# Optimization experiments

Hardware: AMD Instinct MI355X
Metric: run time of the kernel (lower is better)

The kernel has to match this reference:

```python
import jax, jax.numpy as jnp
import numpy as np

B, S, D, H = 4, 1024, 1024, 16
DH = D // H
K_SPARSE = 32
LAMBDA_MAX, ALPHA = 10.0, 5.0
SPARSE_THRESHOLD = 1.0


def setup_inputs() -> dict:
    key = jax.random.key(0)
    ks = jax.random.split(key, 12)
    x = jax.random.normal(ks[0], (B, S, D), dtype=jnp.float32)
    prior_mask = jax.random.bernoulli(ks[1], 0.1, (S, S))
    prior_indices = jax.random.randint(ks[2], (S, K_SPARSE), 0, S)
    prior_index_mask = jax.random.bernoulli(ks[3], 0.9, (S, K_SPARSE))
    prior_index_mask = prior_index_mask.at[:, 0].set(True)  # avoid all-masked rows
    u_prev = jax.random.normal(ks[4], (B, 1), dtype=jnp.float32)
    sc = 1.0 / np.sqrt(D)
    Wq = jax.random.normal(ks[5], (D, D), dtype=jnp.float32) * sc
    Wk = jax.random.normal(ks[6], (D, D), dtype=jnp.float32) * sc
    Wv = jax.random.normal(ks[7], (D, D), dtype=jnp.float32) * sc
    Wo = jax.random.normal(ks[8], (D, D), dtype=jnp.float32) * sc
    bq = jnp.zeros((D,), jnp.float32)
    bk = jnp.zeros((D,), jnp.float32)
    bv = jnp.zeros((D,), jnp.float32)
    bo = jnp.zeros((D,), jnp.float32)
    return {"x": x, "prior_mask": prior_mask, "prior_indices": prior_indices,
            "prior_index_mask": prior_index_mask, "u_prev": u_prev,
            "Wq": Wq, "bq": bq, "Wk": Wk, "bk": bk, "Wv": Wv, "bv": bv,
            "Wo": Wo, "bo": bo}


def reference(x, prior_mask, prior_indices, prior_index_mask, u_prev,
              Wq, bq, Wk, bk, Wv, bv, Wo, bo):
    Bb, Ss, Dd = x.shape
    scale = 1.0 / jnp.sqrt(jnp.asarray(DH, x.dtype))

    def proj(W, b):
        return (x @ W.T + b).reshape(Bb, Ss, H, DH).transpose(0, 2, 1, 3)  # [B,H,S,DH]

    Q, K, V = proj(Wq, bq), proj(Wk, bk), proj(Wv, bv)

    lam = LAMBDA_MAX * jnp.exp(-ALPHA * u_prev.reshape(Bb))  # [B]
    use_sparse = lam >= SPARSE_THRESHOLD                      # [B] bool

    # ---- dense branch: full SDPA with lambda-scaled prior bias ----
    scores = jnp.einsum('bhqd,bhkd->bhqk', Q, K) * scale      # [B,H,S,S]
    prior_bias = jnp.where(prior_mask[:Ss, :Ss], 0.0, -1.0).astype(x.dtype)
    bias = lam[:, None, None, None] * prior_bias[None, None]
    dense_out = jnp.einsum('bhqk,bhkd->bhqd',
                           jax.nn.softmax(scores + bias, axis=-1), V)

    # ---- sparse branch: gather-indexed SDPA over prior_indices ----
    idx = prior_indices[:Ss]                                   # [S,k]
    Kg = K[:, :, idx]                                          # [B,H,S,k,DH]
    Vg = V[:, :, idx]
    s_scores = jnp.einsum('bhsd,bhskd->bhsk', Q, Kg) * scale   # [B,H,S,k]
    s_scores = jnp.where(prior_index_mask[:Ss][None, None], s_scores,
                         jnp.asarray(-jnp.inf, x.dtype))
    sparse_out = jnp.einsum('bhsk,bhskd->bhsd',
                            jax.nn.softmax(s_scores, axis=-1), Vg)

    out = jnp.where(use_sparse[:, None, None, None], sparse_out, dense_out)
    out = out.transpose(0, 2, 1, 3).reshape(Bb, Ss, Dd)
    return out @ Wo.T + bo
```

## Files before the change

### kernel.cpp

```cpp
#include <hip/hip_runtime.h>
#include <hip/hip_bf16.h>
#include <cmath>

#define NB 4
#define NS 1024
#define ND 1024
#define NH 16
#define NDH 64
#define NKSP 32
#define SCALE 0.125f
#define LOG2E 1.44269504f
#define SCALE2 (SCALE * LOG2E)

typedef __attribute__((ext_vector_type(8))) short bf16x8;
typedef __attribute__((ext_vector_type(4))) float f32x4;
typedef unsigned long long u64;

#define AS1 __attribute__((address_space(1)))
#define AS3 __attribute__((address_space(3)))

__device__ __forceinline__ void gl_lds16(const void* g, void* l) {
    __builtin_amdgcn_global_load_lds((const AS1 void*)g, (AS3 void*)l, 16, 0, 0);
}

__device__ __forceinline__ ushort f2bf(float f) {
    union { __hip_bfloat16 h; ushort u; } cv;
    cv.h = __float2bfloat16(f);
    return cv.u;
}
__device__ __forceinline__ float bf2f(ushort u) {
    union { unsigned int i; float f; } cv;
    cv.i = ((unsigned int)u) << 16;
    return cv.f;
}
__device__ __forceinline__ float fexp2(float x) {
    return __builtin_amdgcn_exp2f(x);
}

__global__ __launch_bounds__(256)
void f2bf_multi(const float* __restrict__ x,
                const float* __restrict__ w0, const float* __restrict__ w1,
                const float* __restrict__ w2, const float* __restrict__ w3,
                const int* __restrict__ pm,
                ushort* __restrict__ xo,
                ushort* __restrict__ o0, ushort* __restrict__ o1,
                ushort* __restrict__ o2, ushort* __restrict__ o3,
                u64* __restrict__ bm)
{
    int y = blockIdx.y;
    if (y == 5) {
        int word = blockIdx.x * 4 + (threadIdx.x >> 6);
        int lane = threadIdx.x & 63;
        int row  = word >> 4, wcol = word & 15;
        int v = pm[(size_t)row * NS + wcol * 64 + lane];
        u64 b = __ballot(v != 0);
        if (lane == 0) bm[word] = b;
        return;
    }
    const float* src; ushort* dst; int nblk;
    if (y == 0)      { src = x;  dst = xo; nblk = 4096; }
    else if (y == 1) { src = w0; dst = o0; nblk = 1024; }
    else if (y == 2) { src = w1; dst = o1; nblk = 1024; }
    else if (y == 3) { src = w2; dst = o2; nblk = 1024; }
    else             { src = w3; dst = o3; nblk = 1024; }
    if (blockIdx.x >= (unsigned)nblk) return;
    int i = (blockIdx.x * 256 + threadIdx.x) * 4;
    float4 v = *(const float4*)&src[i];
    ushort4 o;
    o.x = f2bf(v.x); o.y = f2bf(v.y); o.z = f2bf(v.z); o.w = f2bf(v.w);
    *(ushort4*)&dst[i] = o;
}

__global__ __launch_bounds__(256)
void gemm_qkv(const ushort* __restrict__ xb,
              const ushort* __restrict__ Wqb, const ushort* __restrict__ Wkb,
              const ushort* __restrict__ Wvb,
              const float* __restrict__ bq, const float* __restrict__ bk,
              const float* __restrict__ bv,
              ushort* __restrict__ Qo, ushort* __restrict__ Ko,
              ushort* __restrict__ Vo, ushort* __restrict__ Vto)
{
    constexpr int K = ND;
    __shared__ __attribute__((aligned(16))) ushort As[128 * 32];
    __shared__ __attribute__((aligned(16))) ushort Bs[128 * 32];

    const int tid  = threadIdx.x;
    const int lane = tid & 63, w = tid >> 6;
    const int wm = w >> 1, wn = w & 1;
    const int which = blockIdx.x >> 3;
    const int n0 = (blockIdx.x & 7) * 128;
    const int m0 = blockIdx.y * 128;
    const int quad = lane >> 4, l16 = lane & 15;

    const ushort* W = (which == 0) ? Wqb : (which == 1) ? Wkb : Wvb;
    const float* bias = (which == 0) ? bq : (which == 1) ? bk : bv;
    ushort* Out = (which == 0) ? Qo : (which == 1) ? Ko : Vo;

    f32x4 acc[4][4] = {};

    for (int k0 = 0; k0 < K; k0 += 32) {
        __syncthreads();
#pragma unroll
        for (int u = 0; u < 2; ++u) {
            int t0 = u * 256 + w * 64;
            int t  = t0 + lane;
            int row = t >> 2, kc = (t & 3) * 8;
            gl_lds16(xb + (size_t)(m0 + row) * K + k0 + kc, &As[t0 * 8]);
            gl_lds16(W  + (size_t)(n0 + row) * K + k0 + kc, &Bs[t0 * 8]);
        }
        __syncthreads();

        bf16x8 af[4], bfr[4];
#pragma unroll
        for (int mt = 0; mt < 4; ++mt)
            af[mt] = *(const bf16x8*)&As[(wm*64 + mt*16 + l16) * 32 + quad*8];
#pragma unroll
        for (int nt = 0; nt < 4; ++nt)
            bfr[nt] = *(const bf16x8*)&Bs[(wn*64 + nt*16 + l16) * 32 + quad*8];
#pragma unroll
        for (int mt = 0; mt < 4; ++mt)
#pragma unroll
            for (int nt = 0; nt < 4; ++nt)
                acc[mt][nt] = __builtin_amdgcn_mfma_f32_16x16x32_bf16(
                    af[mt], bfr[nt], acc[mt][nt], 0, 0, 0);
    }

#pragma unroll
    for (int nt = 0; nt < 4; ++nt) {
        int n = n0 + wn*64 + nt*16 + l16;
        float bz = bias[n];
        int hh = n >> 6, dh = n & 63;
#pragma unroll
        for (int mt = 0; mt < 4; ++mt) {
#pragma unroll
            for (int rg = 0; rg < 4; ++rg) {
                int m = m0 + wm*64 + mt*16 + quad*4 + rg;
                int b = m >> 10, s = m & (NS - 1);
                ushort val = f2bf(acc[mt][nt][rg] + bz);
                Out[(((size_t)(b*NH + hh))*NS + s)*NDH + dh] = val;
                if (which == 2)
                    Vto[(((size_t)(b*NH + hh))*NDH + dh)*NS + s] = val;
            }
        }
    }
}

__global__ __launch_bounds__(256)
void gemm_out(const ushort* __restrict__ A, const ushort* __restrict__ W,
              const float* __restrict__ bias, float* __restrict__ Cout)
{
    constexpr int K = ND;
    __shared__ __attribute__((aligned(16))) ushort As[64 * 32];
    __shared__ __attribute__((aligned(16))) ushort Bs[128 * 32];

    const int tid  = threadIdx.x;
    const int lane = tid & 63, w = tid >> 6;
    const int wm = w & 1, wn = w >> 1;
    const int m0 = blockIdx.y * 64, n0 = blockIdx.x * 128;
    const int quad = lane >> 4, l16 = lane & 15;

    f32x4 acc[2][4] = {};

    for (int k0 = 0; k0 < K; k0 += 32) {
        __syncthreads();
        {
            int t0 = w * 64;
            int t  = t0 + lane;
            int row = t >> 2, kc = (t & 3) * 8;
            gl_lds16(A + (size_t)(m0 + row) * K + k0 + kc, &As[t0 * 8]);
        }
#pragma unroll
        for (int u = 0; u < 2; ++u) {
            int t0 = u * 256 + w * 64;
            int t  = t0 + lane;
            int row = t >> 2, kc = (t & 3) * 8;
            gl_lds16(W + (size_t)(n0 + row) * K + k0 + kc, &Bs[t0 * 8]);
        }
        __syncthreads();

        bf16x8 af[2], bfr[4];
#pragma unroll
        for (int mt = 0; mt < 2; ++mt)
            af[mt] = *(const bf16x8*)&As[(wm*32 + mt*16 + l16) * 32 + quad*8];
#pragma unroll
        for (int nt = 0; nt < 4; ++nt)
            bfr[nt] = *(const bf16x8*)&Bs[(wn*64 + nt*16 + l16) * 32 + quad*8];
#pragma unroll
        for (int mt = 0; mt < 2; ++mt)
#pragma unroll
            for (int nt = 0; nt < 4; ++nt)
                acc[mt][nt] = __builtin_amdgcn_mfma_f32_16x16x32_bf16(
                    af[mt], bfr[nt], acc[mt][nt], 0, 0, 0);
    }

#pragma unroll
    for (int nt = 0; nt < 4; ++nt) {
        int n = n0 + wn*64 + nt*16 + l16;
        float bz = bias[n];
#pragma unroll
        for (int mt = 0; mt < 2; ++mt) {
#pragma unroll
            for (int rg = 0; rg < 4; ++rg) {
                int m = m0 + wm*32 + mt*16 + quad*4 + rg;
                Cout[(size_t)m * ND + n] = acc[mt][nt][rg] + bz;
            }
        }
    }
}


#define DSTAGE(T4)                                                            \
    _Pragma("unroll")                                                         \
    for (int u = 0; u < 8; ++u) {                                             \
        int cb = w * 512 + u * 64;                                            \
        int c  = cb + lane;                                                   \
        int tk = c >> 9, c2 = c & 511;                                        \
        int row = c2 >> 3, sub = c2 & 7;                                      \
        const ushort* src = Kh + (((size_t)(((T4)*4 + tk)*64 + row)) << 6)    \
                               + ((sub ^ (row & 7)) << 3);                    \
        gl_lds16(src, KK + (size_t)cb * 8);                                   \
    }

#define DLOADKV(KF, VF, KT)                                                   \
    _Pragma("unroll")                                                         \
    for (int nt = 0; nt < 4; ++nt)                                            \
        _Pragma("unroll")                                                     \
        for (int kk = 0; kk < 2; ++kk) {                                      \
            int rowk = nt*16 + l16;                                           \
            int ck = (kk*4 + quad) ^ (l16 & 7);                               \
            KF[nt][kk] = *(const bf16x8*)&KK[w*4096 + rowk*64 + ck*8];        \
            VF[nt][kk] = *(const bf16x8*)                                     \
                &Vth[(size_t)(nt*16 + l16) * NS + (KT)*64 + kk*32 + quad*8];  \
        }

#define DSTEP(KF, VF, M0, M1)                                                 \
    _Pragma("unroll")                                                         \
    for (int qh = 0; qh < 2; ++qh) {                                          \
        const int qrow = qh*16 + l16;                                         \
        u64 wqm = ((qh == 0) ? (M0) : (M1)) >> (quad * 4);                    \
        f32x4 s_acc[4] = {};                                                  \
        __builtin_amdgcn_s_setprio(1);                                        \
        _Pragma("unroll")                                                     \
        for (int nt = 0; nt < 4; ++nt)                                        \
            _Pragma("unroll")                                                 \
            for (int kk = 0; kk < 2; ++kk)                                    \
                s_acc[nt] = __builtin_amdgcn_mfma_f32_16x16x32_bf16(          \
                    KF[nt][kk], qf[qh][kk], s_acc[nt], 0, 0, 0);              \
        __builtin_amdgcn_s_setprio(0);                                        \
        _Pragma("unroll")                                                     \
        for (int nt = 0; nt < 4; ++nt) {                                      \
            ushort4 pk;                                                       \
            float p0 = fexp2(fmaf(s_acc[nt][0], SCALE2,                       \
                 ((wqm >> (nt*16 + 0)) & 1ULL) ? 0.f : nlam2));               \
            float p1 = fexp2(fmaf(s_acc[nt][1], SCALE2,                       \
                 ((wqm >> (nt*16 + 1)) & 1ULL) ? 0.f : nlam2));               \
            float p2 = fexp2(fmaf(s_acc[nt][2], SCALE2,                       \
                 ((wqm >> (nt*16 + 2)) & 1ULL) ? 0.f : nlam2));               \
            float p3 = fexp2(fmaf(s_acc[nt][3], SCALE2,                       \
                 ((wqm >> (nt*16 + 3)) & 1ULL) ? 0.f : nlam2));               \
            pk.x = f2bf(p0); pk.y = f2bf(p1);                                 \
            pk.z = f2bf(p2); pk.w = f2bf(p3);                                 \
            *(ushort4*)&Ps[w*2304 + qrow*72 + nt*16 + quad*4] = pk;           \
        }                                                                     \
        bf16x8 pf[2];                                                         \
        _Pragma("unroll")                                                     \
        for (int kk = 0; kk < 2; ++kk)                                        \
            pf[kk] = *(const bf16x8*)&Ps[w*2304 + qrow*72 + kk*32 + quad*8];  \
        __builtin_amdgcn_s_setprio(1);                                        \
        _Pragma("unroll")                                                     \
        for (int kk = 0; kk < 2; ++kk) {                                      \
            l_acc[qh] = __builtin_amdgcn_mfma_f32_16x16x32_bf16(              \
                pf[kk], ones.v, l_acc[qh], 0, 0, 0);                          \
            _Pragma("unroll")                                                 \
            for (int nt = 0; nt < 4; ++nt)                                    \
                o_acc[qh][nt] = __builtin_amdgcn_mfma_f32_16x16x32_bf16(      \
                    pf[kk], VF[nt][kk], o_acc[qh][nt], 0, 0, 0);              \
        }                                                                     \
        __builtin_amdgcn_s_setprio(0);                                        \
    }

__global__ __launch_bounds__(256)
void attn_dense(const ushort* __restrict__ Qb, const ushort* __restrict__ Kb,
                const ushort* __restrict__ Vt, const u64* __restrict__ bm,
                const float* __restrict__ u_prev, ushort* __restrict__ OA)
{
    __shared__ __attribute__((aligned(16))) ushort SM[25600];
    ushort* KK = SM;
    ushort* Ps = SM + 16384;

    const int tid  = threadIdx.x;
    const int lane = tid & 63, w = tid >> 6;
    const int quad = lane >> 4, l16 = lane & 15;

    float lams[4];
#pragma unroll
    for (int i = 0; i < 4; ++i) lams[i] = 10.0f * __expf(-5.0f * u_prev[i]);
    int dl[4], nd = 0;
#pragma unroll
    for (int i = 0; i < 4; ++i) if (lams[i] < 1.0f) dl[nd++] = i;

    const int id = blockIdx.x;
    if (id >= nd * 512) return;

    int xcd = id & 7, j = id >> 3;
    int nh2 = 2 * nd;
    int hi = j % nh2, qt = j / nh2;
    int gh = hi * 8 + xcd;
    const int b = dl[gh >> 4], h = gh & 15;
    const int s0 = qt * 32;
    const float nlam2 = -lams[b] * LOG2E;

    const size_t bh = (size_t)b * NH + h;
    const ushort* Qh  = Qb + bh * NS * NDH;
    const ushort* Kh  = Kb + bh * NS * NDH;
    const ushort* Vth = Vt + bh * NDH * NS;

    bf16x8 qf[2][2];
#pragma unroll
    for (int qh = 0; qh < 2; ++qh)
#pragma unroll
        for (int kk = 0; kk < 2; ++kk)
            qf[qh][kk] = *(const bf16x8*)
                &Qh[(size_t)(s0 + qh*16 + l16) * NDH + kk*32 + quad*8];

    union { bf16x8 v; ushort s[8]; } ones;
#pragma unroll
    for (int i = 0; i < 8; ++i) ones.s[i] = 0x3F80;

    f32x4 o_acc[2][4] = {};
    f32x4 l_acc[2] = {};

    for (int t = 0; t < 4; ++t) {
        if (t) __syncthreads();
        DSTAGE(t);
        const int kt = 4 * t + w;
        u64 m0 = bm[(size_t)(s0 +  0 + l16) * 16 + kt];
        u64 m1 = bm[(size_t)(s0 + 16 + l16) * 16 + kt];
        __syncthreads();
        bf16x8 kf[4][2], vf[4][2];
        DLOADKV(kf, vf, kt);
        DSTEP(kf, vf, m0, m1);
    }
    __syncthreads();

    float* POUT = (float*)SM;
    if (w != 0) {
        int base = (w - 1) * 2560;
#pragma unroll
        for (int qh = 0; qh < 2; ++qh) {
#pragma unroll
            for (int nt = 0; nt < 4; ++nt)
#pragma unroll
                for (int rg = 0; rg < 4; ++rg)
                    POUT[base + (qh*16 + nt*4 + rg)*64 + lane] =
                        o_acc[qh][nt][rg];
#pragma unroll
            for (int rg = 0; rg < 4; ++rg)
                POUT[base + (32 + qh*4 + rg)*64 + lane] = l_acc[qh][rg];
        }
    }
    __syncthreads();
    if (w == 0) {
#pragma unroll
        for (int s = 0; s < 3; ++s) {
            int base = s * 2560;
#pragma unroll
            for (int qh = 0; qh < 2; ++qh) {
#pragma unroll
                for (int nt = 0; nt < 4; ++nt)
#pragma unroll
                    for (int rg = 0; rg < 4; ++rg)
                        o_acc[qh][nt][rg] +=
                            POUT[base + (qh*16 + nt*4 + rg)*64 + lane];
#pragma unroll
                for (int rg = 0; rg < 4; ++rg)
                    l_acc[qh][rg] += POUT[base + (32 + qh*4 + rg)*64 + lane];
            }
        }
#pragma unroll
        for (int qh = 0; qh < 2; ++qh) {
            float inv[4];
#pragma unroll
            for (int rg = 0; rg < 4; ++rg) inv[rg] = 1.f / l_acc[qh][rg];
#pragma unroll
            for (int nt = 0; nt < 4; ++nt)
#pragma unroll
                for (int rg = 0; rg < 4; ++rg) {
                    int m = qh*16 + quad*4 + rg;
                    OA[((size_t)b*NS + s0 + m)*ND + h*NDH + nt*16 + l16] =
                        f2bf(o_acc[qh][nt][rg] * inv[rg]);
                }
        }
    }
}

__global__ __launch_bounds__(256)
void attn_sparse(const ushort* __restrict__ Qb, const ushort* __restrict__ Kb,
                 const ushort* __restrict__ Vb,
                 const int* __restrict__ pidx, const int* __restrict__ pimask,
                 const float* __restrict__ u_prev, ushort* __restrict__ OA)
{
    const int tid  = threadIdx.x;
    const int lane = tid & 63, w = tid >> 6;
    const int kj = lane >> 3;
    const int c  = lane & 7;

    float lams[4];
#pragma unroll
    for (int i = 0; i < 4; ++i) lams[i] = 10.0f * __expf(-5.0f * u_prev[i]);
    int sl[4], ns = 0;
#pragma unroll
    for (int i = 0; i < 4; ++i) if (lams[i] >= 1.0f) sl[ns++] = i;

    const int id = blockIdx.x;
    if (id >= ns * 1024) return;

    int xcd = id & 7, j = id >> 3;
    int nh2 = 2 * ns;
    int hi = j % nh2, qt = j / nh2;
    int gh = hi * 8 + xcd;
    const int b = sl[gh >> 4], h = gh & 15;
    const int s0 = qt * 16 + w * 4;

    const size_t bh = (size_t)b * NH + h;
    const ushort* Qh = Qb + bh * NS * NDH;
    const ushort* Kh = Kb + bh * NS * NDH;
    const ushort* Vh = Vb + bh * NS * NDH;

    for (int r = 0; r < 4; ++r) {
        const int s = s0 + r;

        float qf[8];
        {
            union { bf16x8 v; ushort u[8]; } qv;
            qv.v = *(const bf16x8*)&Qh[(size_t)s * NDH + c * 8];
#pragma unroll
            for (int e = 0; e < 8; ++e) qf[e] = bf2f(qv.u[e]);
        }

        int kv[4], mv[4];
#pragma unroll
        for (int jj = 0; jj < 4; ++jj) {
            kv[jj] = pidx  [(size_t)s * NKSP + jj*8 + kj];
            mv[jj] = pimask[(size_t)s * NKSP + jj*8 + kj];
        }

        float sc[4];
#pragma unroll
        for (int jj = 0; jj < 4; ++jj) {
            union { bf16x8 v; ushort u[8]; } kc8;
            kc8.v = *(const bf16x8*)&Kh[(size_t)kv[jj] * NDH + c * 8];
            float d = 0.f;
#pragma unroll
            for (int e = 0; e < 8; ++e) d = fmaf(qf[e], bf2f(kc8.u[e]), d);
            d += __shfl_xor(d, 1);
            d += __shfl_xor(d, 2);
            d += __shfl_xor(d, 4);
            sc[jj] = mv[jj] ? d * SCALE : -INFINITY;
        }

        float mt = fmaxf(fmaxf(sc[0], sc[1]), fmaxf(sc[2], sc[3]));
        mt = fmaxf(mt, __shfl_xor(mt, 8));
        mt = fmaxf(mt, __shfl_xor(mt, 16));
        mt = fmaxf(mt, __shfl_xor(mt, 32));

        float p[4], psum = 0.f;
#pragma unroll
        for (int jj = 0; jj < 4; ++jj) {
            p[jj] = __expf(sc[jj] - mt);
            psum += p[jj];
        }
        psum += __shfl_xor(psum, 8);
        psum += __shfl_xor(psum, 16);
        psum += __shfl_xor(psum, 32);

        float o[8];
#pragma unroll
        for (int e = 0; e < 8; ++e) o[e] = 0.f;
#pragma unroll
        for (int jj = 0; jj < 4; ++jj) {
            union { bf16x8 v; ushort u[8]; } vc8;
            vc8.v = *(const bf16x8*)&Vh[(size_t)kv[jj] * NDH + c * 8];
#pragma unroll
            for (int e = 0; e < 8; ++e)
                o[e] = fmaf(p[jj], bf2f(vc8.u[e]), o[e]);
        }
#pragma unroll
        for (int e = 0; e < 8; ++e) {
            o[e] += __shfl_xor(o[e], 8);
            o[e] += __shfl_xor(o[e], 16);
            o[e] += __shfl_xor(o[e], 32);
        }

        if (kj == 0) {
            float inv = 1.f / psum;
            union { bf16x8 v; ushort u[8]; } ov;
#pragma unroll
            for (int e = 0; e < 8; ++e) ov.u[e] = f2bf(o[e] * inv);
            *(bf16x8*)&OA[((size_t)b*NS + s)*ND + h*NDH + c*8] = ov.v;
        }
    }
}

extern "C" void kernel_launch(void* const* d_in, const int* in_sizes, int n_in,
                              void* d_out, int out_size, void* d_ws, size_t ws_size,
                              hipStream_t stream)
{
    const float* x      = (const float*)d_in[0];
    const int*   pmask  = (const int*)  d_in[1];
    const int*   pidx   = (const int*)  d_in[2];
    const int*   pimask = (const int*)  d_in[3];
    const float* u_prev = (const float*)d_in[4];
    const float* Wq     = (const float*)d_in[5];
    const float* bq     = (const float*)d_in[6];
    const float* Wk     = (const float*)d_in[7];
    const float* bk     = (const float*)d_in[8];
    const float* Wv     = (const float*)d_in[9];
    const float* bv     = (const float*)d_in[10];
    const float* Wo     = (const float*)d_in[11];
    const float* bo     = (const float*)d_in[12];
    float* out = (float*)d_out;

    const size_t QSZ = (size_t)NB * NH * NS * NDH;
    const size_t WSZ = (size_t)ND * ND;
    ushort* xb  = (ushort*)d_ws;
    ushort* Qw  = xb  + QSZ;
    ushort* Kw  = Qw  + QSZ;
    ushort* Vw  = Kw  + QSZ;
    ushort* Vtw = Vw  + QSZ;
    ushort* Awb = Vtw + QSZ;
    ushort* Wqb = Awb + QSZ;
    ushort* Wkb = Wqb + WSZ;
    ushort* Wvb = Wkb + WSZ;
    ushort* Wob = Wvb + WSZ;
    u64*    bmw = (u64*)(Wob + WSZ);

    f2bf_multi<<<dim3(4096, 6), 256, 0, stream>>>(
        x, Wq, Wk, Wv, Wo, pmask, xb, Wqb, Wkb, Wvb, Wob, bmw);

    gemm_qkv<<<dim3(24, 32), 256, 0, stream>>>(
        xb, Wqb, Wkb, Wvb, bq, bk, bv, Qw, Kw, Vw, Vtw);

    attn_dense<<<2048, 256, 0, stream>>>(
        Qw, Kw, Vtw, bmw, u_prev, Awb);

    attn_sparse<<<4096, 256, 0, stream>>>(
        Qw, Kw, Vw, pidx, pimask, u_prev, Awb);

    gemm_out<<<dim3(ND/128, (NB*NS)/64), 256, 0, stream>>>(Awb, Wob, bo, out);
}
```

Baseline: 207.0 us.

## Swizzle GEMM LDS tiles and move V transpose into a separate kernel

Applies an XOR swizzle to the LDS tile layout in both the QKV and output GEMMs so that fragment reads by row-strided lanes land in different LDS banks. It also removes the scattered, strided transposed-V store from the QKV GEMM epilogue and adds a dedicated LDS-tiled transpose kernel that writes Vt with vectorized coalesced stores. The trade is an extra kernel launch and an extra read and write of V in exchange for fewer bank conflicts and fewer uncoalesced global writes.

```diff
diff --git a/kernel.cpp b/kernel.cpp
--- a/kernel.cpp
+++ b/kernel.cpp
@@ -78,7 +78,7 @@
               const float* __restrict__ bq, const float* __restrict__ bk,
               const float* __restrict__ bv,
               ushort* __restrict__ Qo, ushort* __restrict__ Ko,
-              ushort* __restrict__ Vo, ushort* __restrict__ Vto)
+              ushort* __restrict__ Vo)
 {
     constexpr int K = ND;
     __shared__ __attribute__((aligned(16))) ushort As[128 * 32];
@@ -104,7 +104,8 @@
         for (int u = 0; u < 2; ++u) {
             int t0 = u * 256 + w * 64;
             int t  = t0 + lane;
-            int row = t >> 2, kc = (t & 3) * 8;
+            int c  = t ^ ((t >> 3) & 7);
+            int row = c >> 2, kc = (c & 3) * 8;
             gl_lds16(xb + (size_t)(m0 + row) * K + k0 + kc, &As[t0 * 8]);
             gl_lds16(W  + (size_t)(n0 + row) * K + k0 + kc, &Bs[t0 * 8]);
         }
@@ -112,11 +113,17 @@
 
         bf16x8 af[4], bfr[4];
 #pragma unroll
-        for (int mt = 0; mt < 4; ++mt)
-            af[mt] = *(const bf16x8*)&As[(wm*64 + mt*16 + l16) * 32 + quad*8];
-#pragma unroll
-        for (int nt = 0; nt < 4; ++nt)
-            bfr[nt] = *(const bf16x8*)&Bs[(wn*64 + nt*16 + l16) * 32 + quad*8];
+        for (int mt = 0; mt < 4; ++mt) {
+            int cidx = (wm*64 + mt*16 + l16)*4 + quad;
+            int p = cidx ^ ((cidx >> 3) & 7);
+            af[mt] = *(const bf16x8*)&As[p * 8];
+        }
+#pragma unroll
+        for (int nt = 0; nt < 4; ++nt) {
+            int cidx = (wn*64 + nt*16 + l16)*4 + quad;
+            int p = cidx ^ ((cidx >> 3) & 7);
+            bfr[nt] = *(const bf16x8*)&Bs[p * 8];
+        }
 #pragma unroll
         for (int mt = 0; mt < 4; ++mt)
 #pragma unroll
@@ -136,12 +143,43 @@
             for (int rg = 0; rg < 4; ++rg) {
                 int m = m0 + wm*64 + mt*16 + quad*4 + rg;
                 int b = m >> 10, s = m & (NS - 1);
-                ushort val = f2bf(acc[mt][nt][rg] + bz);
-                Out[(((size_t)(b*NH + hh))*NS + s)*NDH + dh] = val;
-                if (which == 2)
-                    Vto[(((size_t)(b*NH + hh))*NDH + dh)*NS + s] = val;
+                Out[(((size_t)(b*NH + hh))*NS + s)*NDH + dh] =
+                    f2bf(acc[mt][nt][rg] + bz);
             }
         }
+    }
+}
+
+__global__ __launch_bounds__(256)
+void transpose_v(const ushort* __restrict__ V, ushort* __restrict__ Vt)
+{
+    __shared__ __attribute__((aligned(16))) ushort T[64 * 64];
+
+    const int t  = threadIdx.x;
+    const int bh = blockIdx.x >> 4;
+    const int st = blockIdx.x & 15;
+    const ushort* Vh  = V  + (size_t)bh * NS * NDH + (size_t)st * 64 * NDH;
+    ushort*       Vth = Vt + (size_t)bh * NDH * NS + st * 64;
+
+#pragma unroll
+    for (int i = 0; i < 2; ++i) {
+        int g = i * 256 + t;
+        int srow = g >> 3, sub = g & 7;
+        union { bf16x8 v; ushort u[8]; } x;
+        x.v = *(const bf16x8*)&Vh[(size_t)srow * NDH + sub * 8];
+#pragma unroll
+        for (int e = 0; e < 8; ++e) {
+            int dh = sub * 8 + e;
+            T[dh*64 + (((srow >> 3) ^ sub) * 8) + (srow & 7)] = x.u[e];
+        }
+    }
+    __syncthreads();
+#pragma unroll
+    for (int i = 0; i < 2; ++i) {
+        int g = i * 256 + t;
+        int dh = g >> 3, sc = g & 7;
+        bf16x8 v = *(const bf16x8*)&T[dh*64 + ((sc ^ (dh >> 3)) * 8)];
+        *(bf16x8*)&Vth[(size_t)dh * NS + sc * 8] = v;
     }
 }
 
@@ -166,25 +204,33 @@
         {
             int t0 = w * 64;
             int t  = t0 + lane;
-            int row = t >> 2, kc = (t & 3) * 8;
+            int c  = t ^ ((t >> 3) & 7);
+            int row = c >> 2, kc = (c & 3) * 8;
             gl_lds16(A + (size_t)(m0 + row) * K + k0 + kc, &As[t0 * 8]);
         }
 #pragma unroll
         for (int u = 0; u < 2; ++u) {
             int t0 = u * 256 + w * 64;
             int t  = t0 + lane;
-            int row = t >> 2, kc = (t & 3) * 8;
+            int c  = t ^ ((t >> 3) & 7);
+            int row = c >> 2, kc = (c & 3) * 8;
             gl_lds16(W + (size_t)(n0 + row) * K + k0 + kc, &Bs[t0 * 8]);
         }
         __syncthreads();
 
         bf16x8 af[2], bfr[4];
 #pragma unroll
-        for (int mt = 0; mt < 2; ++mt)
-            af[mt] = *(const bf16x8*)&As[(wm*32 + mt*16 + l16) * 32 + quad*8];
-#pragma unroll
-        for (int nt = 0; nt < 4; ++nt)
-            bfr[nt] = *(const bf16x8*)&Bs[(wn*64 + nt*16 + l16) * 32 + quad*8];
+        for (int mt = 0; mt < 2; ++mt) {
+            int cidx = (wm*32 + mt*16 + l16)*4 + quad;
+            int p = cidx ^ ((cidx >> 3) & 7);
+            af[mt] = *(const bf16x8*)&As[p * 8];
+        }
+#pragma unroll
+        for (int nt = 0; nt < 4; ++nt) {
+            int cidx = (wn*64 + nt*16 + l16)*4 + quad;
+            int p = cidx ^ ((cidx >> 3) & 7);
+            bfr[nt] = *(const bf16x8*)&Bs[p * 8];
+        }
 #pragma unroll
         for (int mt = 0; mt < 2; ++mt)
 #pragma unroll
@@ -207,7 +253,6 @@
         }
     }
 }
-
 
 #define DSTAGE(T4)                                                            \
     _Pragma("unroll")                                                         \
@@ -539,7 +584,9 @@
         x, Wq, Wk, Wv, Wo, pmask, xb, Wqb, Wkb, Wvb, Wob, bmw);
 
     gemm_qkv<<<dim3(24, 32), 256, 0, stream>>>(
-        xb, Wqb, Wkb, Wvb, bq, bk, bv, Qw, Kw, Vw, Vtw);
+        xb, Wqb, Wkb, Wvb, bq, bk, bv, Qw, Kw, Vw);
+
+    transpose_v<<<1024, 256, 0, stream>>>(Vw, Vtw);
 
     attn_dense<<<2048, 256, 0, stream>>>(
         Qw, Kw, Vtw, bmw, u_prev, Awb);
```

After: 203.9 us. About the same (-1.5%).
